# Optimization experiments

Measured on AMD Instinct MI355X. Metric: run time of the kernel, lower is better.

Reference implementation:

```python
import jax, jax.numpy as jnp
import numpy as np

H = 1024      # hidden_size
V = 50257     # output_size (vocab)
L = 512       # max_length (encoder steps)


def setup_inputs() -> dict:
    key = jax.random.key(0)
    ks = jax.random.split(key, 12)
    s = 0.02
    return {
        "input": jax.random.randint(ks[0], (1,), 0, V),
        "h": jax.random.normal(ks[1], (1, 1, H), dtype=jnp.float32),
        "c": jax.random.normal(ks[2], (1, 1, H), dtype=jnp.float32),
        "encoder_outputs": jax.random.normal(ks[3], (L, H), dtype=jnp.float32),
        "emb_table": jax.random.normal(ks[4], (V, H), dtype=jnp.float32) * s,
        "W_attn": jax.random.normal(ks[5], (L, 2 * H), dtype=jnp.float32) * s,
        "b_attn": jnp.zeros((L,), jnp.float32),
        "W_comb": jax.random.normal(ks[6], (H, 2 * H), dtype=jnp.float32) * s,
        "b_comb": jnp.zeros((H,), jnp.float32),
        "W_ih": jax.random.normal(ks[7], (4 * H, H), dtype=jnp.float32) * s,
        "W_hh": jax.random.normal(ks[8], (4 * H, H), dtype=jnp.float32) * s,
        "b_ih": jnp.zeros((4 * H,), jnp.float32),
        "b_hh": jnp.zeros((4 * H,), jnp.float32),
        "W_out": jax.random.normal(ks[9], (V, H), dtype=jnp.float32) * s,
        "b_out": jnp.zeros((V,), jnp.float32),
    }


def reference(input, h, c, encoder_outputs, emb_table, W_attn, b_attn,
              W_comb, b_comb, W_ih, W_hh, b_ih, b_hh, W_out, b_out):
    # Single decode step, batch=1. Dropout is identity (eval mode).
    embedded = emb_table[input]            # [1, H]
    h0 = h[0]                              # [1, H]
    c0 = c[0]                              # [1, H]

    # attention over encoder outputs
    attn_logits = jnp.concatenate([embedded, h0], axis=1) @ W_attn.T + b_attn  # [1, L]
    attn_weights = jax.nn.softmax(attn_logits, axis=1)                          # [1, L]
    attn_applied = attn_weights @ encoder_outputs                               # [1, H]

    # combine + relu
    x = jnp.concatenate([embedded, attn_applied], axis=1) @ W_comb.T + b_comb   # [1, H]
    x = jax.nn.relu(x)

    # single-step LSTM cell (PyTorch gate order: i, f, g, o)
    gates = x @ W_ih.T + b_ih + h0 @ W_hh.T + b_hh                              # [1, 4H]
    i_g, f_g, g_g, o_g = jnp.split(gates, 4, axis=1)
    c1 = jax.nn.sigmoid(f_g) * c0 + jax.nn.sigmoid(i_g) * jnp.tanh(g_g)
    h1 = jax.nn.sigmoid(o_g) * jnp.tanh(c1)

    # output projection + log-softmax
    logp = jax.nn.log_softmax(h1 @ W_out.T + b_out, axis=1)                     # [1, V]
    return (logp, h1[None], c1[None], attn_weights)
```

## Files before the change

kernel.cpp:

```cpp
#include <hip/hip_runtime.h>
#include <math.h>

#define H 1024
#define V 50257
#define L 512

__device__ __forceinline__ float wave_sum(float v) {
#pragma unroll
    for (int off = 32; off; off >>= 1) v += __shfl_xor(v, off, 64);
    return v;
}
__device__ __forceinline__ float wave_max(float v) {
#pragma unroll
    for (int off = 32; off; off >>= 1) v = fmaxf(v, __shfl_xor(v, off, 64));
    return v;
}
__device__ __forceinline__ float sigmoidf(float x) { return 1.f / (1.f + expf(-x)); }

__global__ void k_attn_logits(const int* __restrict__ inp, const float* __restrict__ h0,
                              const float* __restrict__ emb_table,
                              const float* __restrict__ W_attn, const float* __restrict__ b_attn,
                              float* __restrict__ logits) {
    int wave = (blockIdx.x * blockDim.x + threadIdx.x) >> 6;
    int lane = threadIdx.x & 63;
    if (wave >= L) return;
    const float* emb = emb_table + (size_t)inp[0] * H;
    const float* wrow = W_attn + (size_t)wave * (2 * H);
    float acc = 0.f;
#pragma unroll
    for (int it = 0; it < 8; ++it) {
        int k = it * 256 + lane * 4;
        float4 wv = *(const float4*)(wrow + k);
        const float* src = (k < H) ? (emb + k) : (h0 + (k - H));
        float4 xv = *(const float4*)src;
        acc += wv.x * xv.x + wv.y * xv.y + wv.z * xv.z + wv.w * xv.w;
    }
    acc = wave_sum(acc);
    if (lane == 0) logits[wave] = acc + b_attn[wave];
}

__global__ void k_softmax(const float* __restrict__ logits, float* __restrict__ attn_w,
                          float* __restrict__ ws_aa) {
    __shared__ float sh[8];
    __shared__ float bc;
    int t = threadIdx.x, lane = t & 63, wid = t >> 6;
    float v = logits[t];
    float m = wave_max(v);
    if (lane == 0) sh[wid] = m;
    __syncthreads();
    if (t == 0) { float mm = sh[0]; for (int i = 1; i < 8; ++i) mm = fmaxf(mm, sh[i]); bc = mm; }
    __syncthreads();
    m = bc;
    float e = expf(v - m);
    float s = wave_sum(e);
    __syncthreads();
    if (lane == 0) sh[wid] = s;
    __syncthreads();
    if (t == 0) { float ss = 0.f; for (int i = 0; i < 8; ++i) ss += sh[i]; bc = ss; }
    __syncthreads();
    attn_w[t] = e / bc;
    ws_aa[t] = 0.f;
    ws_aa[t + 512] = 0.f;
}

__global__ void k_attn_applied(const float* __restrict__ attn_w, const float* __restrict__ enc,
                               float* __restrict__ ws_aa) {
    int b = blockIdx.x, t = threadIdx.x;
    float4 acc = make_float4(0.f, 0.f, 0.f, 0.f);
#pragma unroll
    for (int r = 0; r < 8; ++r) {
        int l = b * 8 + r;
        float w = attn_w[l];
        float4 e = *(const float4*)(enc + (size_t)l * H + t * 4);
        acc.x += w * e.x; acc.y += w * e.y; acc.z += w * e.z; acc.w += w * e.w;
    }
    atomicAdd(&ws_aa[t * 4 + 0], acc.x);
    atomicAdd(&ws_aa[t * 4 + 1], acc.y);
    atomicAdd(&ws_aa[t * 4 + 2], acc.z);
    atomicAdd(&ws_aa[t * 4 + 3], acc.w);
}

__global__ void k_comb(const int* __restrict__ inp, const float* __restrict__ emb_table,
                       const float* __restrict__ ws_aa, const float* __restrict__ W_comb,
                       const float* __restrict__ b_comb, float* __restrict__ ws_x) {
    int wave = (blockIdx.x * blockDim.x + threadIdx.x) >> 6;
    int lane = threadIdx.x & 63;
    if (wave >= H) return;
    const float* emb = emb_table + (size_t)inp[0] * H;
    const float* wrow = W_comb + (size_t)wave * (2 * H);
    float acc = 0.f;
#pragma unroll
    for (int it = 0; it < 8; ++it) {
        int k = it * 256 + lane * 4;
        float4 wv = *(const float4*)(wrow + k);
        const float* src = (k < H) ? (emb + k) : (ws_aa + (k - H));
        float4 xv = *(const float4*)src;
        acc += wv.x * xv.x + wv.y * xv.y + wv.z * xv.z + wv.w * xv.w;
    }
    acc = wave_sum(acc);
    if (lane == 0) ws_x[wave] = fmaxf(acc + b_comb[wave], 0.f);
}

__global__ void k_gates(const float* __restrict__ ws_x, const float* __restrict__ h0,
                        const float* __restrict__ W_ih, const float* __restrict__ W_hh,
                        const float* __restrict__ b_ih, const float* __restrict__ b_hh,
                        float* __restrict__ gates) {
    int wave = (blockIdx.x * blockDim.x + threadIdx.x) >> 6;
    int lane = threadIdx.x & 63;
    if (wave >= 4 * H) return;
    const float* wi = W_ih + (size_t)wave * H;
    const float* wh = W_hh + (size_t)wave * H;
    float acc = 0.f;
#pragma unroll
    for (int it = 0; it < 4; ++it) {
        int k = it * 256 + lane * 4;
        float4 a = *(const float4*)(wi + k);
        float4 xv = *(const float4*)(ws_x + k);
        acc += a.x * xv.x + a.y * xv.y + a.z * xv.z + a.w * xv.w;
        float4 b = *(const float4*)(wh + k);
        float4 hv = *(const float4*)(h0 + k);
        acc += b.x * hv.x + b.y * hv.y + b.z * hv.z + b.w * hv.w;
    }
    acc = wave_sum(acc);
    if (lane == 0) gates[wave] = acc + b_ih[wave] + b_hh[wave];
}

__global__ void k_lstm(const float* __restrict__ gates, const float* __restrict__ c0,
                       float* __restrict__ out_h1, float* __restrict__ out_c1) {
    int j = threadIdx.x;
    float ig = sigmoidf(gates[j]);
    float fg = sigmoidf(gates[j + H]);
    float gg = tanhf(gates[j + 2 * H]);
    float og = sigmoidf(gates[j + 3 * H]);
    float c1 = fg * c0[j] + ig * gg;
    float h1 = og * tanhf(c1);
    out_c1[j] = c1;
    out_h1[j] = h1;
}

__global__ void k_out(const float* __restrict__ h1, const float* __restrict__ W_out,
                      const float* __restrict__ b_out, float* __restrict__ logp) {
    int wave = (blockIdx.x * blockDim.x + threadIdx.x) >> 6;
    int lane = threadIdx.x & 63;
    if (wave >= V) return;
    const float* wrow = W_out + (size_t)wave * H;
    float acc = 0.f;
#pragma unroll
    for (int it = 0; it < 4; ++it) {
        int k = it * 256 + lane * 4;
        float4 wv = *(const float4*)(wrow + k);
        float4 hv = *(const float4*)(h1 + k);
        acc += wv.x * hv.x + wv.y * hv.y + wv.z * hv.z + wv.w * hv.w;
    }
    acc = wave_sum(acc);
    if (lane == 0) logp[wave] = acc + b_out[wave];
}

__global__ void k_logsoftmax(float* __restrict__ logp) {
    __shared__ float sh[16];
    __shared__ float bc;
    int t = threadIdx.x, lane = t & 63, wid = t >> 6;
    float m = -1e30f;
    for (int v = t; v < V; v += 1024) m = fmaxf(m, logp[v]);
    m = wave_max(m);
    if (lane == 0) sh[wid] = m;
    __syncthreads();
    if (t == 0) { float mm = sh[0]; for (int i = 1; i < 16; ++i) mm = fmaxf(mm, sh[i]); bc = mm; }
    __syncthreads();
    m = bc;
    float s = 0.f;
    for (int v = t; v < V; v += 1024) s += expf(logp[v] - m);
    s = wave_sum(s);
    __syncthreads();
    if (lane == 0) sh[wid] = s;
    __syncthreads();
    if (t == 0) { float ss = 0.f; for (int i = 0; i < 16; ++i) ss += sh[i]; bc = m + logf(ss); }
    __syncthreads();
    float lse = bc;
    for (int v = t; v < V; v += 1024) logp[v] -= lse;
}

extern "C" void kernel_launch(void* const* d_in, const int* in_sizes, int n_in,
                              void* d_out, int out_size, void* d_ws, size_t ws_size,
                              hipStream_t stream) {
    const int*   inp     = (const int*)d_in[0];
    const float* h0      = (const float*)d_in[1];
    const float* c0      = (const float*)d_in[2];
    const float* enc     = (const float*)d_in[3];
    const float* emb     = (const float*)d_in[4];
    const float* W_attn  = (const float*)d_in[5];
    const float* b_attn  = (const float*)d_in[6];
    const float* W_comb  = (const float*)d_in[7];
    const float* b_comb  = (const float*)d_in[8];
    const float* W_ih    = (const float*)d_in[9];
    const float* W_hh    = (const float*)d_in[10];
    const float* b_ih    = (const float*)d_in[11];
    const float* b_hh    = (const float*)d_in[12];
    const float* W_out   = (const float*)d_in[13];
    const float* b_out   = (const float*)d_in[14];

    float* out      = (float*)d_out;
    float* out_logp = out;
    float* out_h1   = out + V;
    float* out_c1   = out + V + H;
    float* out_attn = out + V + 2 * H;

    float* ws        = (float*)d_ws;
    float* ws_logits = ws;
    float* ws_aa     = ws + 512;
    float* ws_x      = ws + 512 + 1024;
    float* ws_gates  = ws + 512 + 2048;

    k_attn_logits<<<128, 256, 0, stream>>>(inp, h0, emb, W_attn, b_attn, ws_logits);
    k_softmax<<<1, 512, 0, stream>>>(ws_logits, out_attn, ws_aa);
    k_attn_applied<<<64, 256, 0, stream>>>(out_attn, enc, ws_aa);
    k_comb<<<256, 256, 0, stream>>>(inp, emb, ws_aa, W_comb, b_comb, ws_x);
    k_gates<<<1024, 256, 0, stream>>>(ws_x, h0, W_ih, W_hh, b_ih, b_hh, ws_gates);
    k_lstm<<<1, 1024, 0, stream>>>(ws_gates, c0, out_h1, out_c1);
    k_out<<<(V + 3) / 4, 256, 0, stream>>>(out_h1, W_out, b_out, out_logp);
    k_logsoftmax<<<1, 1024, 0, stream>>>(out_logp);
}
```

Baseline: 447.8 us.

## Fuse gate GEMV with LSTM cell and parallelize log-softmax across blocks

```diff
diff --git a/kernel.cpp b/kernel.cpp
--- a/kernel.cpp
+++ b/kernel.cpp
@@ -4,6 +4,7 @@
 #define H 1024
 #define V 50257
 #define L 512
+#define RBLK 64
 
 __device__ __forceinline__ float wave_sum(float v) {
 #pragma unroll
@@ -101,15 +102,18 @@
     if (lane == 0) ws_x[wave] = fmaxf(acc + b_comb[wave], 0.f);
 }
 
-__global__ void k_gates(const float* __restrict__ ws_x, const float* __restrict__ h0,
-                        const float* __restrict__ W_ih, const float* __restrict__ W_hh,
-                        const float* __restrict__ b_ih, const float* __restrict__ b_hh,
-                        float* __restrict__ gates) {
-    int wave = (blockIdx.x * blockDim.x + threadIdx.x) >> 6;
-    int lane = threadIdx.x & 63;
-    if (wave >= 4 * H) return;
-    const float* wi = W_ih + (size_t)wave * H;
-    const float* wh = W_hh + (size_t)wave * H;
+__global__ void k_gates_lstm(const float* __restrict__ ws_x, const float* __restrict__ h0,
+                             const float* __restrict__ c0,
+                             const float* __restrict__ W_ih, const float* __restrict__ W_hh,
+                             const float* __restrict__ b_ih, const float* __restrict__ b_hh,
+                             float* __restrict__ out_h1, float* __restrict__ out_c1) {
+    __shared__ float g[4];
+    int j = blockIdx.x;
+    int wv = threadIdx.x >> 6;
+    int lane = threadIdx.x & 63;
+    int row = wv * H + j;
+    const float* wi = W_ih + (size_t)row * H;
+    const float* wh = W_hh + (size_t)row * H;
     float acc = 0.f;
 #pragma unroll
     for (int it = 0; it < 4; ++it) {
@@ -122,20 +126,17 @@
         acc += b.x * hv.x + b.y * hv.y + b.z * hv.z + b.w * hv.w;
     }
     acc = wave_sum(acc);
-    if (lane == 0) gates[wave] = acc + b_ih[wave] + b_hh[wave];
-}
-
-__global__ void k_lstm(const float* __restrict__ gates, const float* __restrict__ c0,
-                       float* __restrict__ out_h1, float* __restrict__ out_c1) {
-    int j = threadIdx.x;
-    float ig = sigmoidf(gates[j]);
-    float fg = sigmoidf(gates[j + H]);
-    float gg = tanhf(gates[j + 2 * H]);
-    float og = sigmoidf(gates[j + 3 * H]);
-    float c1 = fg * c0[j] + ig * gg;
-    float h1 = og * tanhf(c1);
-    out_c1[j] = c1;
-    out_h1[j] = h1;
+    if (lane == 0) g[wv] = acc + b_ih[row] + b_hh[row];
+    __syncthreads();
+    if (threadIdx.x == 0) {
+        float ig = sigmoidf(g[0]);
+        float fg = sigmoidf(g[1]);
+        float gg = tanhf(g[2]);
+        float og = sigmoidf(g[3]);
+        float c1 = fg * c0[j] + ig * gg;
+        out_c1[j] = c1;
+        out_h1[j] = og * tanhf(c1);
+    }
 }
 
 __global__ void k_out(const float* __restrict__ h1, const float* __restrict__ W_out,
@@ -156,28 +157,43 @@
     if (lane == 0) logp[wave] = acc + b_out[wave];
 }
 
-__global__ void k_logsoftmax(float* __restrict__ logp) {
-    __shared__ float sh[16];
-    __shared__ float bc;
+__global__ void k_red(const float* __restrict__ logp, float* __restrict__ pair) {
+    __shared__ float sh[4];
     int t = threadIdx.x, lane = t & 63, wid = t >> 6;
+    float vals[4];
+    int n = 0;
     float m = -1e30f;
-    for (int v = t; v < V; v += 1024) m = fmaxf(m, logp[v]);
+    for (int v = blockIdx.x * 256 + t; v < V; v += RBLK * 256) {
+        vals[n] = logp[v];
+        m = fmaxf(m, vals[n]);
+        ++n;
+    }
     m = wave_max(m);
     if (lane == 0) sh[wid] = m;
     __syncthreads();
-    if (t == 0) { float mm = sh[0]; for (int i = 1; i < 16; ++i) mm = fmaxf(mm, sh[i]); bc = mm; }
-    __syncthreads();
-    m = bc;
+    float m4 = fmaxf(fmaxf(sh[0], sh[1]), fmaxf(sh[2], sh[3]));
     float s = 0.f;
-    for (int v = t; v < V; v += 1024) s += expf(logp[v] - m);
+    for (int i = 0; i < n; ++i) s += expf(vals[i] - m4);
     s = wave_sum(s);
     __syncthreads();
     if (lane == 0) sh[wid] = s;
     __syncthreads();
-    if (t == 0) { float ss = 0.f; for (int i = 0; i < 16; ++i) ss += sh[i]; bc = m + logf(ss); }
-    __syncthreads();
-    float lse = bc;
-    for (int v = t; v < V; v += 1024) logp[v] -= lse;
+    if (t == 0) {
+        pair[blockIdx.x * 2]     = m4;
+        pair[blockIdx.x * 2 + 1] = sh[0] + sh[1] + sh[2] + sh[3];
+    }
+}
+
+__global__ void k_sub(float* __restrict__ logp, const float* __restrict__ pair) {
+    float mg = -1e30f;
+#pragma unroll
+    for (int i = 0; i < RBLK; ++i) mg = fmaxf(mg, pair[2 * i]);
+    float sg = 0.f;
+#pragma unroll
+    for (int i = 0; i < RBLK; ++i) sg += pair[2 * i + 1] * expf(pair[2 * i] - mg);
+    float lse = mg + logf(sg);
+    int v = blockIdx.x * blockDim.x + threadIdx.x;
+    if (v < V) logp[v] -= lse;
 }
 
 extern "C" void kernel_launch(void* const* d_in, const int* in_sizes, int n_in,
@@ -209,14 +225,14 @@
     float* ws_logits = ws;
     float* ws_aa     = ws + 512;
     float* ws_x      = ws + 512 + 1024;
-    float* ws_gates  = ws + 512 + 2048;
+    float* ws_pair   = ws + 512 + 2048;
 
     k_attn_logits<<<128, 256, 0, stream>>>(inp, h0, emb, W_attn, b_attn, ws_logits);
     k_softmax<<<1, 512, 0, stream>>>(ws_logits, out_attn, ws_aa);
     k_attn_applied<<<64, 256, 0, stream>>>(out_attn, enc, ws_aa);
     k_comb<<<256, 256, 0, stream>>>(inp, emb, ws_aa, W_comb, b_comb, ws_x);
-    k_gates<<<1024, 256, 0, stream>>>(ws_x, h0, W_ih, W_hh, b_ih, b_hh, ws_gates);
-    k_lstm<<<1, 1024, 0, stream>>>(ws_gates, c0, out_h1, out_c1);
+    k_gates_lstm<<<1024, 256, 0, stream>>>(ws_x, h0, c0, W_ih, W_hh, b_ih, b_hh, out_h1, out_c1);
     k_out<<<(V + 3) / 4, 256, 0, stream>>>(out_h1, W_out, b_out, out_logp);
-    k_logsoftmax<<<1, 1024, 0, stream>>>(out_logp);
-}
+    k_red<<<RBLK, 256, 0, stream>>>(out_logp, ws_pair);
+    k_sub<<<(V + 255) / 256, 256, 0, stream>>>(out_logp, ws_pair);
+}
```

After: 433.7 us. 3.2% less time.
